# Kernel tuning notes

Measured on AMD Instinct MI355X. Metric: run time of the kernel, lower is better.

The kernel has to match this reference:

```python
import jax, jax.numpy as jnp
import numpy as np

N_NODES = 50000
N_EDGES = 800000
D_IN, D_HID, D_OUT = 128, 128, 256
EPS = 1e-12  # F.normalize eps


def _mean_aggr(h, src, dst, n):
    # scatter-mean of source features onto destination nodes
    msg_sum = jax.ops.segment_sum(h[src], dst, num_segments=n)
    deg = jax.ops.segment_sum(jnp.ones((src.shape[0],), h.dtype), dst, num_segments=n)
    return msg_sum / jnp.maximum(deg, 1.0)[:, None]


def _l2_normalize(h):
    # F.normalize(p=2, dim=1): divide by clamped L2 norm
    nrm = jnp.sqrt(jnp.sum(h * h, axis=1, keepdims=True))
    return h / jnp.maximum(nrm, EPS)


def setup_inputs() -> dict:
    key = jax.random.key(0)
    ks = jax.random.split(key, 8)
    x = jax.random.normal(ks[0], (N_NODES, D_IN), dtype=jnp.float32)
    edge_index = jax.random.randint(ks[1], (2, N_EDGES), 0, N_NODES, dtype=jnp.int64 if jax.config.read('jax_enable_x64') else jnp.int32)
    s = 1.0 / np.sqrt(D_IN)
    W1_l = jax.random.uniform(ks[2], (D_IN, D_HID), jnp.float32, -s, s)
    W1_r = jax.random.uniform(ks[3], (D_IN, D_HID), jnp.float32, -s, s)
    b1 = jnp.zeros((D_HID,), jnp.float32)
    s2 = 1.0 / np.sqrt(D_HID)
    W2_l = jax.random.uniform(ks[4], (D_HID, D_OUT), jnp.float32, -s2, s2)
    W2_r = jax.random.uniform(ks[5], (D_HID, D_OUT), jnp.float32, -s2, s2)
    b2 = jnp.zeros((D_OUT,), jnp.float32)
    return {"x": x, "edge_index": edge_index, "W1_l": W1_l, "W1_r": W1_r,
            "b1": b1, "W2_l": W2_l, "W2_r": W2_r, "b2": b2}


def reference(x, edge_index, W1_l, W1_r, b1, W2_l, W2_r, b2):
    src, dst = edge_index[0], edge_index[1]
    n = x.shape[0]
    # SAGEConv 1: lin_l(mean_aggr(x)) + lin_r(x) + bias
    h = _mean_aggr(x, src, dst, n) @ W1_l + x @ W1_r + b1
    # dropout is identity in eval mode
    h = _l2_normalize(jax.nn.sigmoid(h))
    # SAGEConv 2
    h = _mean_aggr(h, src, dst, n) @ W2_l + h @ W2_r + b2
    h = _l2_normalize(jax.nn.sigmoid(h))
    return jax.nn.log_softmax(h, axis=-1)
```

## Files before the change

kernel.cpp:

```cpp
#include <hip/hip_runtime.h>

#define NN 50000
#define NE 800000
#define NB 782
#define CAP 1536


__device__ __forceinline__ unsigned short f2bf(float f) {
    union { float f; unsigned u; } v; v.f = f;
    unsigned u = v.u;
    return (unsigned short)((u + 0x7fffu + ((u >> 16) & 1u)) >> 16);
}
__device__ __forceinline__ float bfu_lo(unsigned p) {
    union { unsigned u; float f; } v; v.u = p << 16; return v.f;
}
__device__ __forceinline__ float bfu_hi(unsigned p) {
    union { unsigned u; float f; } v; v.u = p & 0xffff0000u; return v.f;
}

typedef __bf16 bf16x8 __attribute__((ext_vector_type(8)));
typedef float f32x4 __attribute__((ext_vector_type(4)));
union U16 { uint4 u; bf16x8 v; };


__global__ __launch_bounds__(512) void binscatter_kernel(const int* __restrict__ src,
                                                         const int* __restrict__ dst,
                                                         int* __restrict__ bcnt,
                                                         unsigned* __restrict__ ebuf) {
    __shared__ int hist[NB];
    __shared__ int base[NB];
    const int BE = 8192;
    int tid = threadIdx.x;
    int e0 = blockIdx.x * BE;
    for (int i = tid; i < NB; i += 512) hist[i] = 0;
    __syncthreads();
    for (int i = tid; i < BE; i += 512) {
        int e = e0 + i;
        if (e < NE) atomicAdd(&hist[dst[e] >> 6], 1);
    }
    __syncthreads();
    for (int i = tid; i < NB; i += 512) {
        int c = hist[i];
        base[i] = c ? atomicAdd(&bcnt[i], c) : 0;
        hist[i] = 0;
    }
    __syncthreads();
    for (int i = tid; i < BE; i += 512) {
        int e = e0 + i;
        if (e < NE) {
            int d = dst[e], b = d >> 6;
            int slot = base[b] + atomicAdd(&hist[b], 1);
            if (slot < CAP)
                ebuf[(size_t)b * CAP + slot] = (unsigned)src[e] | ((unsigned)(d & 63) << 16);
        }
    }
}

__global__ __launch_bounds__(1024) void bscan_kernel(const int* __restrict__ bcnt,
                                                     int* __restrict__ boff,
                                                     int* __restrict__ rowptr) {
    __shared__ int sm[1024];
    int tid = threadIdx.x;
    int v = (tid < NB) ? bcnt[tid] : 0;
    sm[tid] = v;
    __syncthreads();
    for (int off = 1; off < 1024; off <<= 1) {
        int t = (tid >= off) ? sm[tid - off] : 0;
        __syncthreads();
        sm[tid] += t;
        __syncthreads();
    }
    if (tid < NB) boff[tid] = sm[tid] - v;
    if (tid == 0) rowptr[NN] = NE;
}

__global__ __launch_bounds__(256) void csr_kernel(const int* __restrict__ bcnt,
                                                  const int* __restrict__ boff,
                                                  const unsigned* __restrict__ ebuf,
                                                  int* __restrict__ rowptr,
                                                  int* __restrict__ col) {
    __shared__ int deg[64];
    __shared__ int cur[64];
    int b = blockIdx.x, tid = threadIdx.x;
    int cnt = bcnt[b], cbase = boff[b];
    if (tid < 64) deg[tid] = 0;
    __syncthreads();
    const unsigned* eb = ebuf + (size_t)b * CAP;
    for (int i = tid; i < cnt; i += 256) atomicAdd(&deg[eb[i] >> 16], 1);
    __syncthreads();
    if (tid == 0) {
        int run = 0;
        for (int j = 0; j < 64; j++) { cur[j] = run; run += deg[j]; }
    }
    __syncthreads();
    int node = b * 64 + tid;
    if (tid < 64 && node < NN) rowptr[node] = cbase + cur[tid];
    __syncthreads();
    for (int i = tid; i < cnt; i += 256) {
        unsigned e = eb[i];
        int pos = atomicAdd(&cur[e >> 16], 1);
        col[cbase + pos] = (int)(e & 0xffffu);
    }
}


__global__ void cast_bf16_kernel(const float* __restrict__ in, unsigned short* __restrict__ outp,
                                 int n4) {
    int i = blockIdx.x * 256 + threadIdx.x;
    if (i < n4) {
        float4 f = ((const float4*)in)[i];
        ushort4 o;
        o.x = f2bf(f.x); o.y = f2bf(f.y); o.z = f2bf(f.z); o.w = f2bf(f.w);
        ((ushort4*)outp)[i] = o;
    }
}


template <int N>
__global__ void pack_w_kernel(const float* __restrict__ Wl, const float* __restrict__ Wr,
                              unsigned short* __restrict__ Wp) {
    const int NT = N / 16;
    int t = blockIdx.x * 256 + threadIdx.x;
    if (t >= NT * 8 * 64) return;
    int lane = t & 63, c = t >> 6;
    int ks = c & 7, nt = c >> 3;
    int n = nt * 16 + (lane & 15);
    int kq = ks * 32 + (lane >> 4) * 8;
    ushort4 lohi[2];
    unsigned short tmp[8];
#pragma unroll
    for (int j = 0; j < 8; j++) {
        int k = kq + j;
        float w = (k < 128) ? Wl[(size_t)k * N + n] : Wr[(size_t)(k - 128) * N + n];
        tmp[j] = f2bf(w);
    }
    lohi[0] = make_ushort4(tmp[0], tmp[1], tmp[2], tmp[3]);
    lohi[1] = make_ushort4(tmp[4], tmp[5], tmp[6], tmp[7]);
    ((ushort4*)Wp)[(size_t)c * 128 + lane * 2 + 0] = lohi[0];
    ((ushort4*)Wp)[(size_t)c * 128 + lane * 2 + 1] = lohi[1];
}


__global__ void aggregate_bf_kernel(const int* __restrict__ rowptr, const int* __restrict__ col,
                                    const unsigned* __restrict__ feat2,
                                    unsigned* __restrict__ out2) {
    int wid = (blockIdx.x * blockDim.x + threadIdx.x) >> 6;
    int lane = threadIdx.x & 63;
    if (wid >= NN) return;
    int beg = rowptr[wid], end = rowptr[wid + 1];
    float ax = 0.f, ay = 0.f;
    int i = beg;
    for (; i + 4 <= end; i += 4) {
        int s0 = col[i], s1 = col[i + 1], s2 = col[i + 2], s3 = col[i + 3];
        unsigned v0 = feat2[s0 * 64 + lane], v1 = feat2[s1 * 64 + lane];
        unsigned v2 = feat2[s2 * 64 + lane], v3 = feat2[s3 * 64 + lane];
        ax += bfu_lo(v0) + bfu_lo(v1) + bfu_lo(v2) + bfu_lo(v3);
        ay += bfu_hi(v0) + bfu_hi(v1) + bfu_hi(v2) + bfu_hi(v3);
    }
    for (; i < end; i++) {
        unsigned v = feat2[col[i] * 64 + lane];
        ax += bfu_lo(v); ay += bfu_hi(v);
    }
    float inv = (end > beg) ? 1.0f / (float)(end - beg) : 0.0f;
    unsigned o = (unsigned)f2bf(ax * inv) | ((unsigned)f2bf(ay * inv) << 16);
    out2[wid * 64 + lane] = o;
}


template <int N, bool FINAL>
__global__ __launch_bounds__(256) void gemm_mfma_kernel(
    const unsigned short* __restrict__ A0, const unsigned short* __restrict__ A1,
    const unsigned short* __restrict__ Wp, const float* __restrict__ bias,
    void* __restrict__ outp, int M) {
    const int NT = N / 16;
    int tid = threadIdx.x, wave = tid >> 6, lane = tid & 63;
    int quad = lane >> 4, col = lane & 15;
    int m_base = blockIdx.x * 64 + wave * 16;
    int row = m_base + col;
    int row_ld = row < M ? row : M - 1;

    bf16x8 a[8];
    const uint4* a0p = (const uint4*)(A0 + (size_t)row_ld * 128 + quad * 8);
    const uint4* a1p = (const uint4*)(A1 + (size_t)row_ld * 128 + quad * 8);
#pragma unroll
    for (int ks = 0; ks < 4; ks++) { U16 u; u.u = a0p[ks * 4]; a[ks] = u.v; }
#pragma unroll
    for (int ks = 0; ks < 4; ks++) { U16 u; u.u = a1p[ks * 4]; a[4 + ks] = u.v; }

    f32x4 acc[NT];
#pragma unroll
    for (int nt = 0; nt < NT; nt++) acc[nt] = (f32x4){0.f, 0.f, 0.f, 0.f};

    const uint4* wp = (const uint4*)Wp;
#pragma unroll
    for (int nt = 0; nt < NT; nt++) {
#pragma unroll
        for (int ks = 0; ks < 8; ks++) {
            U16 u; u.u = wp[(size_t)(nt * 8 + ks) * 64 + lane];
            acc[nt] = __builtin_amdgcn_mfma_f32_16x16x32_bf16(a[ks], u.v, acc[nt], 0, 0, 0);
        }
    }

    float ssq[4] = {0.f, 0.f, 0.f, 0.f};
#pragma unroll
    for (int nt = 0; nt < NT; nt++) {
        float bv = bias[nt * 16 + col];
#pragma unroll
        for (int r = 0; r < 4; r++) {
            float z = acc[nt][r] + bv;
            float s = 1.0f / (1.0f + __expf(-z));
            acc[nt][r] = s;
            ssq[r] += s * s;
        }
    }
#pragma unroll
    for (int r = 0; r < 4; r++) {
#pragma unroll
        for (int off = 1; off < 16; off <<= 1) ssq[r] += __shfl_xor(ssq[r], off, 16);
        float sc = 1.0f / fmaxf(sqrtf(ssq[r]), 1e-12f);
#pragma unroll
        for (int nt = 0; nt < NT; nt++) acc[nt][r] *= sc;
    }

    if (FINAL) {
#pragma unroll
        for (int r = 0; r < 4; r++) {
            float mx = -1e30f;
#pragma unroll
            for (int nt = 0; nt < NT; nt++) mx = fmaxf(mx, acc[nt][r]);
#pragma unroll
            for (int off = 1; off < 16; off <<= 1) mx = fmaxf(mx, __shfl_xor(mx, off, 16));
            float se = 0.f;
#pragma unroll
            for (int nt = 0; nt < NT; nt++) se += __expf(acc[nt][r] - mx);
#pragma unroll
            for (int off = 1; off < 16; off <<= 1) se += __shfl_xor(se, off, 16);
            float lse = mx + __logf(se);
#pragma unroll
            for (int nt = 0; nt < NT; nt++) acc[nt][r] -= lse;
        }
        float* op = (float*)outp;
#pragma unroll
        for (int r = 0; r < 4; r++) {
            int m = m_base + quad * 4 + r;
            if (m < M) {
#pragma unroll
                for (int nt = 0; nt < NT; nt++) op[(size_t)m * N + nt * 16 + col] = acc[nt][r];
            }
        }
    } else {
        unsigned short* op = (unsigned short*)outp;
#pragma unroll
        for (int r = 0; r < 4; r++) {
            int m = m_base + quad * 4 + r;
            if (m < M) {
#pragma unroll
                for (int nt = 0; nt < NT; nt++)
                    op[(size_t)m * N + nt * 16 + col] = f2bf(acc[nt][r]);
            }
        }
    }
}


extern "C" void kernel_launch(void* const* d_in, const int* in_sizes, int n_in,
                              void* d_out, int out_size, void* d_ws, size_t ws_size,
                              hipStream_t stream) {
    const float* x   = (const float*)d_in[0];
    const int*   ei  = (const int*)d_in[1];
    const float* W1l = (const float*)d_in[2];
    const float* W1r = (const float*)d_in[3];
    const float* b1  = (const float*)d_in[4];
    const float* W2l = (const float*)d_in[5];
    const float* W2r = (const float*)d_in[6];
    const float* b2  = (const float*)d_in[7];
    float* out = (float*)d_out;

    const int* src = ei;
    const int* dst = ei + NE;

    char* ws = (char*)d_ws;
    size_t off = 0;
    auto alloc = [&](size_t bytes) -> void* {
        void* p = ws + off;
        off += (bytes + 255) / 256 * 256;
        return p;
    };
    int* rowptr     = (int*)alloc((size_t)(NN + 1) * 4);
    int* col        = (int*)alloc((size_t)NE * 4);
    int* bcnt       = (int*)alloc((size_t)NB * 4);
    int* boff       = (int*)alloc((size_t)NB * 4);
    unsigned* ebuf  = (unsigned*)alloc((size_t)NB * CAP * 4);
    unsigned short* x_bf   = (unsigned short*)alloc((size_t)NN * 128 * 2);
    unsigned short* agg_bf = (unsigned short*)alloc((size_t)NN * 128 * 2);
    unsigned short* h1_bf  = (unsigned short*)alloc((size_t)NN * 128 * 2);
    unsigned short* W1p    = (unsigned short*)alloc((size_t)8 * 8 * 64 * 8 * 2);
    unsigned short* W2p    = (unsigned short*)alloc((size_t)16 * 8 * 64 * 8 * 2);

    hipMemsetAsync(bcnt, 0, (size_t)NB * 4, stream);
    binscatter_kernel<<<(NE + 8191) / 8192, 512, 0, stream>>>(src, dst, bcnt, ebuf);
    bscan_kernel<<<1, 1024, 0, stream>>>(bcnt, boff, rowptr);
    csr_kernel<<<NB, 256, 0, stream>>>(bcnt, boff, ebuf, rowptr, col);

    cast_bf16_kernel<<<(NN * 128 / 4 + 255) / 256, 256, 0, stream>>>(x, x_bf, NN * 128 / 4);
    pack_w_kernel<128><<<(8 * 8 * 64 + 255) / 256, 256, 0, stream>>>(W1l, W1r, W1p);
    pack_w_kernel<256><<<(16 * 8 * 64 + 255) / 256, 256, 0, stream>>>(W2l, W2r, W2p);

    aggregate_bf_kernel<<<(NN + 3) / 4, 256, 0, stream>>>(rowptr, col, (const unsigned*)x_bf,
                                                          (unsigned*)agg_bf);
    gemm_mfma_kernel<128, false><<<(NN + 63) / 64, 256, 0, stream>>>(agg_bf, x_bf, W1p, b1,
                                                                     h1_bf, NN);
    aggregate_bf_kernel<<<(NN + 3) / 4, 256, 0, stream>>>(rowptr, col, (const unsigned*)h1_bf,
                                                          (unsigned*)agg_bf);
    gemm_mfma_kernel<256, true><<<(NN + 63) / 64, 256, 0, stream>>>(agg_bf, h1_bf, W2p, b2,
                                                                    out, NN);
}
```

Before: 259.3 us.

## Vectorize aggregation with 16-byte loads, fold bucket scan into CSR kernel

The aggregation kernel now has each wave process four edges at a time. Each group of 16 lanes fetches a full 256-byte row with uint4 loads and accumulates eight bf16 lanes, and the four partial sums are then reduced with cross-lane shuffles. This targets gather efficiency and memory-level parallelism in the two dominant aggregation passes. The separate single-block bucket scan kernel is removed: each CSR block now computes its own offset by summing the preceding bucket counts, which costs some redundant reads. The two weight-packing launches are also merged into one. These last two changes cut kernel launch count.

```diff
diff --git a/kernel.cpp b/kernel.cpp
--- a/kernel.cpp
+++ b/kernel.cpp
@@ -56,37 +56,30 @@
     }
 }
 
-__global__ __launch_bounds__(1024) void bscan_kernel(const int* __restrict__ bcnt,
-                                                     int* __restrict__ boff,
-                                                     int* __restrict__ rowptr) {
-    __shared__ int sm[1024];
-    int tid = threadIdx.x;
-    int v = (tid < NB) ? bcnt[tid] : 0;
-    sm[tid] = v;
-    __syncthreads();
-    for (int off = 1; off < 1024; off <<= 1) {
-        int t = (tid >= off) ? sm[tid - off] : 0;
-        __syncthreads();
-        sm[tid] += t;
-        __syncthreads();
-    }
-    if (tid < NB) boff[tid] = sm[tid] - v;
-    if (tid == 0) rowptr[NN] = NE;
-}
-
 __global__ __launch_bounds__(256) void csr_kernel(const int* __restrict__ bcnt,
-                                                  const int* __restrict__ boff,
                                                   const unsigned* __restrict__ ebuf,
                                                   int* __restrict__ rowptr,
                                                   int* __restrict__ col) {
+    __shared__ int red[256];
     __shared__ int deg[64];
     __shared__ int cur[64];
+    __shared__ int cbase_s;
     int b = blockIdx.x, tid = threadIdx.x;
-    int cnt = bcnt[b], cbase = boff[b];
+    int s = 0;
+    for (int i = tid; i < b; i += 256) s += bcnt[i];
+    red[tid] = s;
     if (tid < 64) deg[tid] = 0;
     __syncthreads();
+    for (int off = 128; off; off >>= 1) {
+        if (tid < off) red[tid] += red[tid + off];
+        __syncthreads();
+    }
+    if (tid == 0) cbase_s = red[0];
+    __syncthreads();
+    int cnt = bcnt[b], cbase = cbase_s;
+    if (cnt > CAP) cnt = CAP;
     const unsigned* eb = ebuf + (size_t)b * CAP;
-    for (int i = tid; i < cnt; i += 256) atomicAdd(&deg[eb[i] >> 16], 1);
+    for (int i = tid; i < cnt; i += 256) atomicAdd(&deg[(eb[i] >> 16) & 63], 1);
     __syncthreads();
     if (tid == 0) {
         int run = 0;
@@ -95,10 +88,11 @@
     __syncthreads();
     int node = b * 64 + tid;
     if (tid < 64 && node < NN) rowptr[node] = cbase + cur[tid];
+    if (b == NB - 1 && tid == 0) rowptr[NN] = NE;
     __syncthreads();
     for (int i = tid; i < cnt; i += 256) {
         unsigned e = eb[i];
-        int pos = atomicAdd(&cur[e >> 16], 1);
+        int pos = atomicAdd(&cur[(e >> 16) & 63], 1);
         col[cbase + pos] = (int)(e & 0xffffu);
     }
 }
@@ -117,16 +111,13 @@
 
 
 template <int N>
-__global__ void pack_w_kernel(const float* __restrict__ Wl, const float* __restrict__ Wr,
-                              unsigned short* __restrict__ Wp) {
-    const int NT = N / 16;
-    int t = blockIdx.x * 256 + threadIdx.x;
-    if (t >= NT * 8 * 64) return;
+__device__ __forceinline__ void pack_one(const float* __restrict__ Wl,
+                                         const float* __restrict__ Wr,
+                                         unsigned short* __restrict__ Wp, int t) {
     int lane = t & 63, c = t >> 6;
     int ks = c & 7, nt = c >> 3;
     int n = nt * 16 + (lane & 15);
     int kq = ks * 32 + (lane >> 4) * 8;
-    ushort4 lohi[2];
     unsigned short tmp[8];
 #pragma unroll
     for (int j = 0; j < 8; j++) {
@@ -134,36 +125,56 @@
         float w = (k < 128) ? Wl[(size_t)k * N + n] : Wr[(size_t)(k - 128) * N + n];
         tmp[j] = f2bf(w);
     }
-    lohi[0] = make_ushort4(tmp[0], tmp[1], tmp[2], tmp[3]);
-    lohi[1] = make_ushort4(tmp[4], tmp[5], tmp[6], tmp[7]);
-    ((ushort4*)Wp)[(size_t)c * 128 + lane * 2 + 0] = lohi[0];
-    ((ushort4*)Wp)[(size_t)c * 128 + lane * 2 + 1] = lohi[1];
+    ((ushort4*)Wp)[(size_t)c * 128 + lane * 2 + 0] = make_ushort4(tmp[0], tmp[1], tmp[2], tmp[3]);
+    ((ushort4*)Wp)[(size_t)c * 128 + lane * 2 + 1] = make_ushort4(tmp[4], tmp[5], tmp[6], tmp[7]);
+}
+
+__global__ void pack_both_kernel(const float* __restrict__ W1l, const float* __restrict__ W1r,
+                                 unsigned short* __restrict__ W1p,
+                                 const float* __restrict__ W2l, const float* __restrict__ W2r,
+                                 unsigned short* __restrict__ W2p) {
+    int t = blockIdx.x * 256 + threadIdx.x;
+    if (t < 8 * 8 * 64) pack_one<128>(W1l, W1r, W1p, t);
+    else if (t < 8 * 8 * 64 + 16 * 8 * 64) pack_one<256>(W2l, W2r, W2p, t - 8 * 8 * 64);
 }
 
 
 __global__ void aggregate_bf_kernel(const int* __restrict__ rowptr, const int* __restrict__ col,
-                                    const unsigned* __restrict__ feat2,
-                                    unsigned* __restrict__ out2) {
+                                    const uint4* __restrict__ feat4,
+                                    uint4* __restrict__ out4) {
     int wid = (blockIdx.x * blockDim.x + threadIdx.x) >> 6;
     int lane = threadIdx.x & 63;
     if (wid >= NN) return;
     int beg = rowptr[wid], end = rowptr[wid + 1];
-    float ax = 0.f, ay = 0.f;
-    int i = beg;
-    for (; i + 4 <= end; i += 4) {
-        int s0 = col[i], s1 = col[i + 1], s2 = col[i + 2], s3 = col[i + 3];
-        unsigned v0 = feat2[s0 * 64 + lane], v1 = feat2[s1 * 64 + lane];
-        unsigned v2 = feat2[s2 * 64 + lane], v3 = feat2[s3 * 64 + lane];
-        ax += bfu_lo(v0) + bfu_lo(v1) + bfu_lo(v2) + bfu_lo(v3);
-        ay += bfu_hi(v0) + bfu_hi(v1) + bfu_hi(v2) + bfu_hi(v3);
-    }
-    for (; i < end; i++) {
-        unsigned v = feat2[col[i] * 64 + lane];
-        ax += bfu_lo(v); ay += bfu_hi(v);
-    }
-    float inv = (end > beg) ? 1.0f / (float)(end - beg) : 0.0f;
-    unsigned o = (unsigned)f2bf(ax * inv) | ((unsigned)f2bf(ay * inv) << 16);
-    out2[wid * 64 + lane] = o;
+    int g = lane >> 4, c16 = lane & 15;
+    float acc[8];
+#pragma unroll
+    for (int j = 0; j < 8; j++) acc[j] = 0.f;
+    for (int i = beg; i < end; i += 4) {
+        int idx = i + g;
+        if (idx < end) {
+            int s = col[idx];
+            uint4 v = feat4[(size_t)s * 16 + c16];
+            acc[0] += bfu_lo(v.x); acc[1] += bfu_hi(v.x);
+            acc[2] += bfu_lo(v.y); acc[3] += bfu_hi(v.y);
+            acc[4] += bfu_lo(v.z); acc[5] += bfu_hi(v.z);
+            acc[6] += bfu_lo(v.w); acc[7] += bfu_hi(v.w);
+        }
+    }
+#pragma unroll
+    for (int j = 0; j < 8; j++) {
+        acc[j] += __shfl_xor(acc[j], 16);
+        acc[j] += __shfl_xor(acc[j], 32);
+    }
+    if (g == 0) {
+        float inv = (end > beg) ? 1.0f / (float)(end - beg) : 0.0f;
+        uint4 o;
+        o.x = (unsigned)f2bf(acc[0] * inv) | ((unsigned)f2bf(acc[1] * inv) << 16);
+        o.y = (unsigned)f2bf(acc[2] * inv) | ((unsigned)f2bf(acc[3] * inv) << 16);
+        o.z = (unsigned)f2bf(acc[4] * inv) | ((unsigned)f2bf(acc[5] * inv) << 16);
+        o.w = (unsigned)f2bf(acc[6] * inv) | ((unsigned)f2bf(acc[7] * inv) << 16);
+        out4[(size_t)wid * 16 + c16] = o;
+    }
 }
 
 
@@ -289,7 +300,6 @@
     int* rowptr     = (int*)alloc((size_t)(NN + 1) * 4);
     int* col        = (int*)alloc((size_t)NE * 4);
     int* bcnt       = (int*)alloc((size_t)NB * 4);
-    int* boff       = (int*)alloc((size_t)NB * 4);
     unsigned* ebuf  = (unsigned*)alloc((size_t)NB * CAP * 4);
     unsigned short* x_bf   = (unsigned short*)alloc((size_t)NN * 128 * 2);
     unsigned short* agg_bf = (unsigned short*)alloc((size_t)NN * 128 * 2);
@@ -299,19 +309,17 @@
 
     hipMemsetAsync(bcnt, 0, (size_t)NB * 4, stream);
     binscatter_kernel<<<(NE + 8191) / 8192, 512, 0, stream>>>(src, dst, bcnt, ebuf);
-    bscan_kernel<<<1, 1024, 0, stream>>>(bcnt, boff, rowptr);
-    csr_kernel<<<NB, 256, 0, stream>>>(bcnt, boff, ebuf, rowptr, col);
+    csr_kernel<<<NB, 256, 0, stream>>>(bcnt, ebuf, rowptr, col);
 
     cast_bf16_kernel<<<(NN * 128 / 4 + 255) / 256, 256, 0, stream>>>(x, x_bf, NN * 128 / 4);
-    pack_w_kernel<128><<<(8 * 8 * 64 + 255) / 256, 256, 0, stream>>>(W1l, W1r, W1p);
-    pack_w_kernel<256><<<(16 * 8 * 64 + 255) / 256, 256, 0, stream>>>(W2l, W2r, W2p);
-
-    aggregate_bf_kernel<<<(NN + 3) / 4, 256, 0, stream>>>(rowptr, col, (const unsigned*)x_bf,
-                                                          (unsigned*)agg_bf);
+    pack_both_kernel<<<(24 * 8 * 64 + 255) / 256, 256, 0, stream>>>(W1l, W1r, W1p, W2l, W2r, W2p);
+
+    aggregate_bf_kernel<<<(NN + 3) / 4, 256, 0, stream>>>(rowptr, col, (const uint4*)x_bf,
+                                                          (uint4*)agg_bf);
     gemm_mfma_kernel<128, false><<<(NN + 63) / 64, 256, 0, stream>>>(agg_bf, x_bf, W1p, b1,
                                                                      h1_bf, NN);
-    aggregate_bf_kernel<<<(NN + 3) / 4, 256, 0, stream>>>(rowptr, col, (const unsigned*)h1_bf,
-                                                          (unsigned*)agg_bf);
+    aggregate_bf_kernel<<<(NN + 3) / 4, 256, 0, stream>>>(rowptr, col, (const uint4*)h1_bf,
+                                                          (uint4*)agg_bf);
     gemm_mfma_kernel<256, true><<<(NN + 63) / 64, 256, 0, stream>>>(agg_bf, h1_bf, W2p, b2,
                                                                     out, NN);
 }
```

Result: faster. 253.4 us (-2.3%).
